# Performance work log

Measured on AMD Instinct MI355X. Metric: run time of the kernel, lower is better.

Reference implementation:

```python
import jax, jax.numpy as jnp
import numpy as np

NUM_HEADS = 16
NUM_KV_HEADS = 4
ROPE_BASE = 10000.0
TRAIN_SEQ_LEN = 2048


def _rms_norm(x):
    eps = jnp.asarray(jnp.finfo(x.dtype).eps, x.dtype)
    return x * jax.lax.rsqrt(jnp.mean(x * x, axis=-1, keepdims=True) + eps)


def _rope_cos_sin(seq_len, head_dim, dtype):
    # seq_len <= TRAIN_SEQ_LEN -> no NTK rescaling, matches Rotary buffer path
    half = head_dim // 2
    inv_freq = 1.0 / (ROPE_BASE ** (jnp.arange(0, head_dim, 2, dtype=jnp.float32) / head_dim))
    t = jnp.arange(seq_len, dtype=jnp.float32)
    freqs = jnp.outer(t, inv_freq)  # [S, half]
    cos = jnp.cos(freqs)[None, :, None, :].astype(dtype)
    sin = jnp.sin(freqs)[None, :, None, :].astype(dtype)
    return cos, sin


def _apply_rotary(x, cos, sin):
    half = x.shape[-1] // 2
    x1, x2 = x[..., :half], x[..., half:]
    return jnp.concatenate([x1 * cos + x2 * sin, -x1 * sin + x2 * cos], axis=-1)


def setup_inputs() -> dict:
    key = jax.random.key(0)
    ks = jax.random.split(key, 5)
    B, S, D = 2, 2048, 2048
    kv_dim = NUM_KV_HEADS * (D // NUM_HEADS)
    sw = 0.02
    return {
        "x": jax.random.normal(ks[0], (B, S, D), jnp.float32),
        "Wq": jax.random.normal(ks[1], (D, D), jnp.float32) * sw,
        "Wk": jax.random.normal(ks[2], (kv_dim, D), jnp.float32) * sw,
        "Wv": jax.random.normal(ks[3], (kv_dim, D), jnp.float32) * sw,
        "Wproj": jax.random.normal(ks[4], (D, D), jnp.float32) * sw,
        "q_gain": jnp.ones((NUM_HEADS,), jnp.float32),
    }


def reference(x, Wq, Wk, Wv, Wproj, q_gain):
    B, S, D = x.shape
    H, Hkv = NUM_HEADS, NUM_KV_HEADS
    hd = D // H
    r = H // Hkv

    q = (x @ Wq.T).reshape(B, S, H, hd)
    k = (x @ Wk.T).reshape(B, S, Hkv, hd)
    v = (x @ Wv.T).reshape(B, S, Hkv, hd)

    q = _rms_norm(q)
    k = _rms_norm(k)

    cos, sin = _rope_cos_sin(S, hd, q.dtype)
    q = _apply_rotary(q, cos, sin)
    k = _apply_rotary(k, cos, sin)
    q = q * q_gain.astype(q.dtype)[None, None, :, None]

    # GQA: repeat kv heads (repeat_interleave along head dim)
    k = jnp.repeat(k, r, axis=2)  # [B,S,H,hd]
    v = jnp.repeat(v, r, axis=2)

    scale = 1.0 / jnp.sqrt(jnp.asarray(hd, q.dtype))
    scores = jnp.einsum("bqhd,bkhd->bhqk", q, k) * scale
    causal = jnp.tril(jnp.ones((S, S), dtype=bool))
    scores = jnp.where(causal[None, None], scores, jnp.asarray(-jnp.inf, scores.dtype))
    attn = jax.nn.softmax(scores, axis=-1)
    y = jnp.einsum("bhqk,bkhd->bqhd", attn, v)

    return y.reshape(B, S, D) @ Wproj.T
```

## Files before the change

kernel.cpp:

```cpp
#include <hip/hip_runtime.h>

#define D_MODEL 2048
#define SEQ 2048
#define BATCH 2
#define NH 16
#define NKV 4
#define HD 128
#define KVD (NKV * HD)
#define QKVN (D_MODEL + 2 * KVD)
#define MROWS (BATCH * SEQ)

typedef __attribute__((ext_vector_type(8))) short short8;
typedef __attribute__((ext_vector_type(4))) float f32x4;

__device__ __forceinline__ unsigned short f2bf(float f) {
    union { float f; unsigned int u; } v; v.f = f;
    unsigned int r = (v.u + 0x7FFFu + ((v.u >> 16) & 1u)) >> 16;
    return (unsigned short)r;
}

__device__ __forceinline__ unsigned short f2bf_pos(float f) {
    union { float f; unsigned int u; } v; v.f = f;
    return (unsigned short)((v.u + 0x8000u) >> 16);
}

__device__ __forceinline__ float bf2f(unsigned short u) {
    union { float f; unsigned int i; } v; v.i = ((unsigned int)u) << 16;
    return v.f;
}

__device__ __forceinline__ void async16(const void* g, void* l) {
    __builtin_amdgcn_global_load_lds((const __attribute__((address_space(1))) void*)g,
                                     (__attribute__((address_space(3))) void*)l, 16, 0, 0);
}

__global__ __launch_bounds__(256) void cast_all(const float* __restrict__ x,
                                                const float* __restrict__ wq,
                                                const float* __restrict__ wk,
                                                const float* __restrict__ wv,
                                                const float* __restrict__ wp,
                                                unsigned short* __restrict__ xb,
                                                unsigned short* __restrict__ wqkv,
                                                unsigned short* __restrict__ wpb) {
    int i = blockIdx.x * 256 + threadIdx.x;
    const float4* s; ushort4* d; int j;
    if (i < 2097152)      { s = (const float4*)x;  d = (ushort4*)xb;             j = i; }
    else if (i < 3145728) { s = (const float4*)wq; d = (ushort4*)wqkv;           j = i - 2097152; }
    else if (i < 3407872) { s = (const float4*)wk; d = (ushort4*)wqkv + 1048576; j = i - 3145728; }
    else if (i < 3670016) { s = (const float4*)wv; d = (ushort4*)wqkv + 1310720; j = i - 3407872; }
    else                  { s = (const float4*)wp; d = (ushort4*)wpb;            j = i - 3670016; }
    float4 v = s[j];
    ushort4 o;
    o.x = f2bf(v.x); o.y = f2bf(v.y); o.z = f2bf(v.z); o.w = f2bf(v.w);
    d[j] = o;
}

__global__ __launch_bounds__(512) void gemm_qkv(const unsigned short* __restrict__ A,
                                                const unsigned short* __restrict__ W,
                                                const float* __restrict__ gain,
                                                unsigned short* __restrict__ qbuf,
                                                unsigned short* __restrict__ kbuf,
                                                unsigned short* __restrict__ vtb) {
    __shared__ unsigned short smem[65536];
    unsigned short* tile = smem;
    const int K = D_MODEL;
    const int tid  = threadIdx.x;
    const int lane = tid & 63;
    const int wave = tid >> 6;
    const int qm   = lane & 15;
    const int quad = lane >> 4;
    const int wr   = wave >> 2;
    const int wc   = wave & 3;
    const int lin = blockIdx.x + 12 * blockIdx.y;
    const int l2  = (lin & 7) * 24 + (lin >> 3);
    const int bx  = l2 % 12;
    const int m0  = (l2 / 12) * 256;
    const int n0 = bx * 256;

    f32x4 acc[2][2][4][2];
#pragma unroll
    for (int a = 0; a < 2; a++)
#pragma unroll
        for (int b = 0; b < 2; b++)
#pragma unroll
            for (int c = 0; c < 4; c++)
#pragma unroll
                for (int d = 0; d < 2; d++) acc[a][b][c][d] = (f32x4){0.f, 0.f, 0.f, 0.f};

    const unsigned short* Asrc = A + (size_t)(m0 + (tid >> 3)) * K + (((tid & 7) ^ ((tid >> 3) & 7)) * 8);
    const unsigned short* Bsrc = W + (size_t)(n0 + (tid >> 3)) * K + (((tid & 7) ^ ((tid >> 3) & 7)) * 8);
    const int dstg = tid * 8;
    const int ck0 = ((quad ^ (qm & 7)) * 8);
    const int ck1 = (((4 + quad) ^ (qm & 7)) * 8);
    const int arow = wr * 64 + qm;
    const int brow = wc * 32 + qm;

    short8 af[4][2], bf0[2][2], bf1[2][2];

#define STG_A(mh, bufv, kt1) \
    async16(Asrc + (size_t)((mh) * 128) * K + (kt1),      &smem[(bufv) * 16384 + (mh) * 8192 + dstg]); \
    async16(Asrc + (size_t)((mh) * 128 + 64) * K + (kt1), &smem[(bufv) * 16384 + (mh) * 8192 + 4096 + dstg]);
#define STG_B(nh, bufv, kt1) \
    async16(Bsrc + (size_t)((nh) * 128) * K + (kt1),      &smem[32768 + (bufv) * 16384 + (nh) * 8192 + dstg]); \
    async16(Bsrc + (size_t)((nh) * 128 + 64) * K + (kt1), &smem[32768 + (bufv) * 16384 + (nh) * 8192 + 4096 + dstg]);

#define RD_A(ab, mh) { \
    _Pragma("unroll") \
    for (int m = 0; m < 4; m++) { \
        af[m][0] = *(const short8*)&smem[(ab) + ((mh) * 128 + arow + m * 16) * 64 + ck0]; \
        af[m][1] = *(const short8*)&smem[(ab) + ((mh) * 128 + arow + m * 16) * 64 + ck1]; \
    } }
#define RD_B(bb, nh, dstf) { \
    _Pragma("unroll") \
    for (int n = 0; n < 2; n++) { \
        dstf[n][0] = *(const short8*)&smem[(bb) + ((nh) * 128 + brow + n * 16) * 64 + ck0]; \
        dstf[n][1] = *(const short8*)&smem[(bb) + ((nh) * 128 + brow + n * 16) * 64 + ck1]; \
    } }
#define MFMA16(mh, nh, bfr) { \
    __builtin_amdgcn_s_setprio(1); \
    _Pragma("unroll") \
    for (int m = 0; m < 4; m++) \
        _Pragma("unroll") \
        for (int n = 0; n < 2; n++) { \
            acc[mh][nh][m][n] = __builtin_amdgcn_mfma_f32_16x16x32_bf16(af[m][0], bfr[n][0], acc[mh][nh][m][n], 0, 0, 0); \
            acc[mh][nh][m][n] = __builtin_amdgcn_mfma_f32_16x16x32_bf16(af[m][1], bfr[n][1], acc[mh][nh][m][n], 0, 0, 0); \
        } \
    __builtin_amdgcn_s_setprio(0); }

#define BARv asm volatile("s_barrier" ::: "memory")
#define WV4  asm volatile("s_waitcnt vmcnt(4)" ::: "memory")
#define WV2  asm volatile("s_waitcnt vmcnt(2)" ::: "memory")
#define WV0  asm volatile("s_waitcnt vmcnt(0)" ::: "memory")

#define STEP(p, kt1) { \
     RD_A((p)*16384, 0) RD_B(32768 + (p)*16384, 0, bf0) STG_A(0, (p)^1, kt1) \
    BARv; MFMA16(0, 0, bf0) WV4; BARv; \
     RD_B(32768 + (p)*16384, 1, bf1) STG_B(0, (p)^1, kt1) \
    BARv; MFMA16(0, 1, bf1) WV4; BARv; \
     RD_A((p)*16384, 1) STG_B(1, (p)^1, kt1) \
    BARv; MFMA16(1, 0, bf0) BARv; \
     STG_A(1, (p)^1, kt1) \
    BARv; MFMA16(1, 1, bf1) WV4; BARv; \
}
#define STEPE(p) { \
    RD_A((p)*16384, 0) RD_B(32768 + (p)*16384, 0, bf0) BARv; MFMA16(0, 0, bf0) WV2; BARv; \
    RD_B(32768 + (p)*16384, 1, bf1)                    BARv; MFMA16(0, 1, bf1) WV0; BARv; \
    RD_A((p)*16384, 1)                                 BARv; MFMA16(1, 0, bf0) BARv; \
    MFMA16(1, 1, bf1) \
}

    STG_A(0, 0, 0) STG_B(0, 0, 0) STG_B(1, 0, 0) STG_A(1, 0, 0)
    WV4; BARv;

#pragma unroll 1
    for (int t2 = 0; t2 < 15; ++t2) {
        STEP(0, t2 * 128 + 64)
        STEP(1, t2 * 128 + 128)
    }
    STEP(0, 1984)
    STEPE(1)
#undef STG_A
#undef STG_B
#undef RD_A
#undef RD_B
#undef MFMA16
#undef STEP
#undef STEPE

    const int s_base = m0 & 2047;
    const int bb = m0 >> 11;
    const float invf = __builtin_amdgcn_exp2f(-(float)lane * 0.20761871f - 2.6514961f);

#pragma unroll
    for (int half = 0; half < 2; ++half) {
        __syncthreads();
#pragma unroll
        for (int nh = 0; nh < 2; nh++)
#pragma unroll
            for (int m = 0; m < 4; m++)
#pragma unroll
                for (int n = 0; n < 2; n++)
#pragma unroll
                    for (int r = 0; r < 4; r++) {
                        int row = wr * 64 + m * 16 + quad * 4 + r;
                        int col = nh * 128 + wc * 32 + n * 16 + qm;
                        tile[row * 264 + col] = f2bf(acc[half][nh][m][n][r]);
                    }
        __syncthreads();

        if (bx < 10) {
            const bool isq = bx < 8;
#pragma unroll
            for (int hh = 0; hh < 2; hh++) {
                const int h = (isq ? 2 * bx : (bx - 8) * 2) + hh;
                const float g = isq ? gain[h] * 0.12751744f : 1.0f;
                unsigned short* dst = isq
                    ? qbuf + ((size_t)(bb * NH + h) * SEQ + s_base + half * 128) * HD
                    : kbuf + ((size_t)(bb * NKV + h) * SEQ + s_base + half * 128) * HD;
                for (int rr = 0; rr < 16; rr++) {
                    int row = wave * 16 + rr;
                    float x1 = bf2f(tile[row * 264 + hh * 128 + lane]);
                    float x2 = bf2f(tile[row * 264 + hh * 128 + 64 + lane]);
                    float ss = x1 * x1 + x2 * x2;
                    ss += __shfl_xor(ss, 1);  ss += __shfl_xor(ss, 2);  ss += __shfl_xor(ss, 4);
                    ss += __shfl_xor(ss, 8);  ss += __shfl_xor(ss, 16); ss += __shfl_xor(ss, 32);
                    float rs = rsqrtf(ss * (1.0f / 128.0f) + 1.1920929e-07f);
                    float rev = (float)(s_base + half * 128 + row) * invf;
                    rev -= truncf(rev);
                    float sn = __builtin_amdgcn_sinf(rev);
                    float cs = __builtin_amdgcn_cosf(rev);
                    float a1 = x1 * rs, a2 = x2 * rs;
                    float o1 = (a1 * cs + a2 * sn) * g;
                    float o2 = (a2 * cs - a1 * sn) * g;
                    dst[(size_t)row * HD + lane]      = f2bf(o1);
                    dst[(size_t)row * HD + 64 + lane] = f2bf(o2);
                }
            }
        } else {
            const int sc = (tid & 31) * 4;
            const int d0 = tid >> 5;
#pragma unroll
            for (int hh = 0; hh < 2; hh++) {
                const int hk = (bx - 10) * 2 + hh;
                unsigned short* dstv = vtb + ((size_t)(bb * NKV + hk) * HD) * SEQ + s_base + half * 128;
#pragma unroll
                for (int i = 0; i < 8; i++) {
                    int d = d0 + 16 * i;
                    ushort4 ov;
                    ov.x = tile[(sc + 0) * 264 + hh * 128 + d];
                    ov.y = tile[(sc + 1) * 264 + hh * 128 + d];
                    ov.z = tile[(sc + 2) * 264 + hh * 128 + d];
                    ov.w = tile[(sc + 3) * 264 + hh * 128 + d];
                    *(ushort4*)(dstv + (size_t)d * SEQ + sc) = ov;
                }
            }
        }
    }
}

__global__ __launch_bounds__(256) void gemm_bt(const unsigned short* __restrict__ A,
                                               const unsigned short* __restrict__ W,
                                               float* __restrict__ C, int M, int N, int K) {
    __shared__ unsigned short smem[32768];
    unsigned short* Al = smem;
    unsigned short* Bl = smem + 16384;
    const int tid  = threadIdx.x;
    const int lane = tid & 63;
    const int wave = tid >> 6;
    const int qm   = lane & 15;
    const int quad = lane >> 4;
    const int m0 = blockIdx.y * 128;
    const int n0 = blockIdx.x * 128;
    const int wm = (wave >> 1) * 64;
    const int wn = (wave & 1) * 64;

    f32x4 acc[4][4];
#pragma unroll
    for (int i = 0; i < 4; i++)
#pragma unroll
        for (int j = 0; j < 4; j++) acc[i][j] = (f32x4){0.f, 0.f, 0.f, 0.f};

    const int r1 = tid >> 2;
    const int c1 = (((tid & 3) ^ ((tid >> 3) & 3)) * 8);
    const unsigned short* Ag = A + (size_t)(m0 + r1) * K + c1;
    const unsigned short* Wg = W + (size_t)(n0 + r1) * K + c1;
    const int stg = wave * 512;
    const int swq = ((qm >> 1) & 3) * 8;

#define STG_B2(khv, bufv) \
    async16(Ag + (khv) * 32,                  &Al[(bufv) * 8192 + (khv) * 4096 + stg]); \
    async16(Ag + (khv) * 32 + (size_t)64 * K, &Al[(bufv) * 8192 + (khv) * 4096 + 2048 + stg]); \
    async16(Wg + (khv) * 32,                  &Bl[(bufv) * 8192 + (khv) * 4096 + stg]); \
    async16(Wg + (khv) * 32 + (size_t)64 * K, &Bl[(bufv) * 8192 + (khv) * 4096 + 2048 + stg]);

#define CMP_B2(bufv, khv) { \
    short8 af[4], bfr[4]; \
    _Pragma("unroll") \
    for (int i = 0; i < 4; i++) { \
        af[i]  = *(const short8*)&Al[(bufv) * 8192 + (khv) * 4096 + (wm + i * 16 + qm) * 32 + (quad * 8 ^ swq)]; \
        bfr[i] = *(const short8*)&Bl[(bufv) * 8192 + (khv) * 4096 + (wn + i * 16 + qm) * 32 + (quad * 8 ^ swq)]; \
    } \
    __builtin_amdgcn_s_setprio(1); \
    _Pragma("unroll") \
    for (int mi = 0; mi < 4; mi++) \
        _Pragma("unroll") \
        for (int ni = 0; ni < 4; ni++) \
            acc[mi][ni] = __builtin_amdgcn_mfma_f32_16x16x32_bf16(af[mi], bfr[ni], acc[mi][ni], 0, 0, 0); \
    __builtin_amdgcn_s_setprio(0); \
}

    STG_B2(0, 0)
    STG_B2(1, 0)
    Ag += 64; Wg += 64;
    asm volatile("s_waitcnt vmcnt(4)\n\ts_barrier" ::: "memory");

    int buf = 0;
    for (int t = 0; t < K / 64 - 1; ++t) {
        STG_B2(0, buf ^ 1)
        CMP_B2(buf, 0)
        asm volatile("s_waitcnt vmcnt(4)\n\ts_barrier" ::: "memory");
        STG_B2(1, buf ^ 1)
        CMP_B2(buf, 1)
        asm volatile("s_waitcnt vmcnt(4)\n\ts_barrier" ::: "memory");
        Ag += 64; Wg += 64;
        buf ^= 1;
    }
    CMP_B2(buf, 0)
    asm volatile("s_waitcnt vmcnt(0)\n\ts_barrier" ::: "memory");
    CMP_B2(buf, 1)
#undef STG_B2
#undef CMP_B2

#pragma unroll
    for (int mi = 0; mi < 4; mi++) {
#pragma unroll
        for (int r = 0; r < 4; r++) {
            int row = m0 + wm + mi * 16 + quad * 4 + r;
            float* Crow = C + (size_t)row * N + n0 + wn + qm;
#pragma unroll
            for (int ni = 0; ni < 4; ni++) Crow[ni * 16] = acc[mi][ni][r];
        }
    }
}

__global__ __launch_bounds__(256, 4) void attn(const unsigned short* __restrict__ qb,
                                               const unsigned short* __restrict__ kb,
                                               const unsigned short* __restrict__ vt,
                                               const float* __restrict__ gain,
                                               unsigned short* __restrict__ y) {
    __shared__ unsigned short Ks[8192];
    __shared__ unsigned short Vs[8192];
    __shared__ unsigned short plds[4][1024];
    const int tid  = threadIdx.x;
    const int lane = tid & 63;
    const int wave = tid >> 6;
    const int bh   = blockIdx.x & 31;
    const int g4   = blockIdx.x >> 5;
    const int gg = g4 & 7;
    const int gs = g4 >> 3;
    const int qt64 = (gs == 0) ? gg : (gs == 1) ? (31 - gg) : (gs == 2) ? (8 + gg) : (23 - gg);
    const int h = bh & 15;
    const int b = bh >> 4;
    const int qm   = lane & 15;
    const int quad = lane >> 4;
    const int q0    = qt64 * 64;
    const int qrow0 = q0 + wave * 16;
    const float M = 17.0f * fabsf(gain[h]);

    const unsigned short* Qp = qb + (((size_t)(b * NH + h)) * SEQ + qrow0) * HD;
    const unsigned short* Kp = kb + ((size_t)(b * NKV + (h >> 2))) * SEQ * HD;
    const unsigned short* Vp = vt + ((size_t)(b * NKV + (h >> 2))) * HD * SEQ;

    short8 qf[4];
#pragma unroll
    for (int c = 0; c < 4; c++)
        qf[c] = *(const short8*)(Qp + qm * HD + c * 32 + quad * 8);

    f32x4 o[8];
#pragma unroll
    for (int t = 0; t < 8; t++) o[t] = (f32x4){0.f, 0.f, 0.f, 0.f};
    float lr[4] = {0.f, 0.f, 0.f, 0.f};

    const unsigned short* KsA = Kp + (size_t)(tid >> 4) * HD + (((tid & 15) ^ (tid >> 4)) & 15) * 8;
    const unsigned short* VsA = Vp + (size_t)(tid >> 3) * SEQ + (((tid & 7) ^ ((tid >> 3) & 7)) * 8);
    char* KsB = (char*)Ks + wave * 1024;
    char* VsB = (char*)Vs + wave * 1024;
    unsigned short* P = &plds[wave][0];

    const int kvend = q0 + 64;
    for (int kv0 = 0; kv0 < kvend; kv0 += 64) {
#pragma unroll
        for (int i = 0; i < 4; i++) {
            async16(KsA + (size_t)(16 * i) * HD,  KsB + i * 4096);
            async16(VsA + (size_t)(32 * i) * SEQ, VsB + i * 4096);
        }
        KsA += (size_t)64 * HD;
        VsA += 64;
        __syncthreads();

        f32x4 s[4];
#pragma unroll
        for (int g = 0; g < 4; g++) s[g] = (f32x4){0.f, 0.f, 0.f, 0.f};
#pragma unroll
        for (int c = 0; c < 4; c++) {
#pragma unroll
            for (int g = 0; g < 4; g++) {
                short8 kf = *(const short8*)&Ks[(g * 16 + qm) * 128 + (((c * 4 + quad) ^ qm) * 8)];
                s[g] = __builtin_amdgcn_mfma_f32_16x16x32_bf16(qf[c], kf, s[g], 0, 0, 0);
            }
        }
        if (kv0 + 63 > qrow0) {
#pragma unroll
            for (int g = 0; g < 4; g++)
#pragma unroll
                for (int r = 0; r < 4; r++) {
                    int qg = qrow0 + quad * 4 + r;
                    if (kv0 + g * 16 + qm > qg) s[g][r] = -3.0e38f;
                }
        }
        float p[4][4];
#pragma unroll
        for (int g = 0; g < 4; g++)
#pragma unroll
            for (int r = 0; r < 4; r++) {
                p[g][r] = __builtin_amdgcn_exp2f(s[g][r] - M);
                lr[r] += p[g][r];
            }
#pragma unroll
        for (int g = 0; g < 4; g++)
#pragma unroll
            for (int r = 0; r < 4; r++) {
                int rowp = quad * 4 + r;
                P[rowp * 64 + (((g * 2 + (qm >> 3)) ^ (rowp & 7)) * 8) + (qm & 7)] = f2bf_pos(p[g][r]);
            }
        short8 pa[2];
#pragma unroll
        for (int ka = 0; ka < 2; ka++)
            pa[ka] = *(const short8*)&P[qm * 64 + (((ka * 4 + quad) ^ (qm & 7)) * 8)];
#pragma unroll
        for (int t = 0; t < 8; t++) {
#pragma unroll
            for (int ka = 0; ka < 2; ka++) {
                short8 vf = *(const short8*)&Vs[(t * 16 + qm) * 64 + (((ka * 4 + quad) ^ (qm & 7)) * 8)];
                o[t] = __builtin_amdgcn_mfma_f32_16x16x32_bf16(pa[ka], vf, o[t], 0, 0, 0);
            }
        }
        __syncthreads();
    }
    float rl[4];
#pragma unroll
    for (int r = 0; r < 4; r++) {
        float l = lr[r];
        l += __shfl_xor(l, 1);
        l += __shfl_xor(l, 2);
        l += __shfl_xor(l, 4);
        l += __shfl_xor(l, 8);
        rl[r] = 1.0f / l;
    }
#pragma unroll
    for (int t = 0; t < 8; t++) {
#pragma unroll
        for (int r = 0; r < 4; r++) {
            size_t row = (size_t)(b * SEQ + qrow0 + quad * 4 + r);
            y[row * D_MODEL + h * HD + t * 16 + qm] = f2bf(o[t][r] * rl[r]);
        }
    }
}

extern "C" void kernel_launch(void* const* d_in, const int* in_sizes, int n_in,
                              void* d_out, int out_size, void* d_ws, size_t ws_size,
                              hipStream_t stream) {
    const float* x  = (const float*)d_in[0];
    const float* Wq = (const float*)d_in[1];
    const float* Wk = (const float*)d_in[2];
    const float* Wv = (const float*)d_in[3];
    const float* Wp = (const float*)d_in[4];
    const float* qg = (const float*)d_in[5];

    char* ws = (char*)d_ws;
    unsigned short* xb   = (unsigned short*)(ws + 0);
    unsigned short* wqkv = (unsigned short*)(ws + 16777216);
    unsigned short* wp   = (unsigned short*)(ws + 29360128);
    unsigned short* qbuf = (unsigned short*)(ws + 37748736);
    unsigned short* kbuf = (unsigned short*)(ws + 54525952);
    unsigned short* vtb  = (unsigned short*)(ws + 58720256);
    unsigned short* y    = xb;

    cast_all<<<18432, 256, 0, stream>>>(x, Wq, Wk, Wv, Wp, xb, wqkv, wp);
    gemm_qkv<<<dim3(12, 16), 512, 0, stream>>>(xb, wqkv, qg, qbuf, kbuf, vtb);
    attn<<<1024, 256, 0, stream>>>(qbuf, kbuf, vtb, qg, y);
    gemm_bt<<<dim3(16, 32), 256, 0, stream>>>(y, wp, (float*)d_out, MROWS, D_MODEL, D_MODEL);
}
```

Baseline: 284.8 us.

## Prefetch next K/V tile into registers during attention compute

Replaces the async global-to-LDS copies for K and V tiles with register prefetching. The next tile is loaded into registers while the current tile is being computed, then written to LDS between two barriers. This is meant to hide global memory latency behind the MFMA work. In exchange it raises register pressure and relies on raw s_barrier without explicit waitcnt, which could risk ordering issues or lower occupancy.

```diff
diff --git a/kernel.cpp b/kernel.cpp
--- a/kernel.cpp
+++ b/kernel.cpp
@@ -363,20 +363,33 @@
 
     const unsigned short* KsA = Kp + (size_t)(tid >> 4) * HD + (((tid & 15) ^ (tid >> 4)) & 15) * 8;
     const unsigned short* VsA = Vp + (size_t)(tid >> 3) * SEQ + (((tid & 7) ^ ((tid >> 3) & 7)) * 8);
-    char* KsB = (char*)Ks + wave * 1024;
-    char* VsB = (char*)Vs + wave * 1024;
+    const int dst8 = tid * 8;
     unsigned short* P = &plds[wave][0];
+
+    short8 kreg[4], vreg[4];
+#define LD_KV() { \
+    _Pragma("unroll") \
+    for (int i = 0; i < 4; i++) { \
+        kreg[i] = *(const short8*)(KsA + (size_t)(16 * i) * HD); \
+        vreg[i] = *(const short8*)(VsA + (size_t)(32 * i) * SEQ); \
+    } \
+    KsA += (size_t)64 * HD; \
+    VsA += 64; }
+#define WR_KV() { \
+    _Pragma("unroll") \
+    for (int i = 0; i < 4; i++) { \
+        *(short8*)&Ks[i * 2048 + dst8] = kreg[i]; \
+        *(short8*)&Vs[i * 2048 + dst8] = vreg[i]; \
+    } }
+
+    LD_KV()
+    WR_KV()
+    __syncthreads();
 
     const int kvend = q0 + 64;
     for (int kv0 = 0; kv0 < kvend; kv0 += 64) {
-#pragma unroll
-        for (int i = 0; i < 4; i++) {
-            async16(KsA + (size_t)(16 * i) * HD,  KsB + i * 4096);
-            async16(VsA + (size_t)(32 * i) * SEQ, VsB + i * 4096);
-        }
-        KsA += (size_t)64 * HD;
-        VsA += 64;
-        __syncthreads();
+        const bool more = (kv0 + 64 < kvend);
+        if (more) LD_KV()
 
         f32x4 s[4];
 #pragma unroll
@@ -425,8 +438,12 @@
                 o[t] = __builtin_amdgcn_mfma_f32_16x16x32_bf16(pa[ka], vf, o[t], 0, 0, 0);
             }
         }
-        __syncthreads();
-    }
+        asm volatile("s_barrier" ::: "memory");
+        if (more) WR_KV()
+        asm volatile("s_barrier" ::: "memory");
+    }
+#undef LD_KV
+#undef WR_KV
     float rl[4];
 #pragma unroll
     for (int r = 0; r < 4; r++) {
```

After: 375.6 us. 31.9% more time.
